# Kernel tuning notes

Hardware: AMD Instinct MI355X
Metric: run time of the kernel (lower is better)

Reference implementation:

```python
import jax, jax.numpy as jnp
import numpy as np


def setup_inputs() -> dict:
    key = jax.random.key(0)
    ks = jax.random.split(key, 8)
    B, T, I, H, O = 4096, 2048, 4, 20, 4
    s_ih = 1.0 / np.sqrt(H)
    return {
        "x": jax.random.normal(ks[0], (B, T, I), dtype=jnp.float32),
        "h0": jax.random.normal(ks[1], (B, H), dtype=jnp.float32),
        "W_ih": jax.random.uniform(ks[2], (H, I), jnp.float32, -s_ih, s_ih),
        "W_hh": jax.random.uniform(ks[3], (H, H), jnp.float32, -s_ih, s_ih),
        "b_ih": jax.random.uniform(ks[4], (H,), jnp.float32, -s_ih, s_ih),
        "b_hh": jax.random.uniform(ks[5], (H,), jnp.float32, -s_ih, s_ih),
        "fc_w": jax.random.uniform(ks[6], (O, H), jnp.float32, -s_ih, s_ih),
        "fc_b": jax.random.uniform(ks[7], (O,), jnp.float32, -s_ih, s_ih),
    }


def reference(x, h0, W_ih, W_hh, b_ih, b_hh, fc_w, fc_b):
    # x: [B, T, I] batch_first; vanilla tanh RNN recurrence.
    # Precompute the input projection for all timesteps in one GEMM.
    xi = jnp.einsum("bti,hi->tbh", x, W_ih) + b_ih + b_hh  # [T, B, H]

    def step(h, xt):
        h = jnp.tanh(xt + h @ W_hh.T)  # [B, H]
        return h, None

    h_last, _ = jax.lax.scan(step, h0, xi)
    # Module takes last timestep only, then Linear(H -> 4).
    return h_last @ fc_w.T + fc_b  # [B, 4]
```

## Files before the change

kernel.cpp:

```cpp
#include <hip/hip_runtime.h>
#include <cstddef>


typedef float f32x2 __attribute__((ext_vector_type(2)));
typedef float f32x4 __attribute__((ext_vector_type(4)));

constexpr int Tn   = 2048;
constexpr int Hn   = 20;
constexpr int EPB  = 16;
constexpr int SB   = 16;
constexpr int NBLK = Tn / SB;

__global__ __launch_bounds__(256, 1) void rnn_fwd(
    const float* __restrict__ x,
    const float* __restrict__ h0,
    const float* __restrict__ W_ih,
    const float* __restrict__ W_hh,
    const float* __restrict__ b_ih,
    const float* __restrict__ b_hh,
    const float* __restrict__ fc_w,
    const float* __restrict__ fc_b,
    float* __restrict__ out)
{
    __shared__ __align__(16) f32x4 xlds[2][EPB][SB + 1];
    __shared__ float hsh[EPB][24];

    const int tid = threadIdx.x;
    const int j   = tid & 15;
    const int e   = tid >> 4;
    const int b   = blockIdx.x * EPB + e;
    const int uB  = 16 + (j & 3);

    const float S = 2.88539008177792681472f;
    const float M = -2.0f * S;

    f32x2 w2[16];
#pragma unroll
    for (int r = 0; r < 16; ++r) {
        const int k = (j - r) & 15;
        w2[r] = f32x2{M * W_hh[j * Hn + k], M * W_hh[uB * Hn + k]};
    }
    f32x2 wqr[4], xiw[4];
#pragma unroll
    for (int c = 0; c < 4; ++c) {
        const int qc = 16 + ((j + c) & 3);
        wqr[c] = f32x2{M * W_hh[j * Hn + qc], M * W_hh[uB * Hn + qc]};
        xiw[c] = f32x2{S * W_ih[j * 4 + c],  S * W_ih[uB * 4 + c]};
    }
    float rsA = 0.0f, rsB = 0.0f;
#pragma unroll
    for (int k = 0; k < Hn; ++k) {
        rsA += W_hh[j  * Hn + k];
        rsB += W_hh[uB * Hn + k];
    }
    f32x2 bias2 = f32x2{S * (b_ih[j]  + b_hh[j]  + rsA),
                        S * (b_ih[uB] + b_hh[uB] + rsB)};

    const float r0A = 0.5f * (1.0f - h0[b * Hn + j]);
    const float r0B = 0.5f * (1.0f - h0[b * Hn + uB]);

    const f32x4* __restrict__ xp =
        reinterpret_cast<const f32x4*>(x) + (size_t)b * Tn;

#define DPPM " row_mask:0xf bank_mask:0xf\n\t"
#define PKB  " op_sel:[0,0,0] op_sel_hi:[1,0,1]\n\t"
#define CLB  "v40","v41","v42","v43","v44","v45","v46","v47","v48","v49",     \
             "v50","v51","v52","v53"

#define STEP_MAC() do {                                                       \
    asm volatile(                                                             \
  "v_pk_fma_f32 %[Q], %[c0], v[44:45], %[Q]" PKB             \
  "v_mov_b32_dpp v42, v44 quad_perm:[1,2,3,0]" DPPM                           \
  "v_pk_fma_f32 %[P], %[w0], v[40:41], %[P]" PKB              \
  "v_mov_b32_dpp v46, v44 quad_perm:[2,3,0,1]" DPPM                           \
  "v_pk_fma_f32 %[Q], %[c1], v[42:43], %[Q]" PKB                              \
  "v_mov_b32_dpp v48, v44 quad_perm:[3,0,1,2]" DPPM                           \
  "v_pk_fma_f32 %[P], %[c2], v[46:47], %[P]" PKB                              \
  "v_mov_b32_dpp v42, v40 row_ror:1"  DPPM                                    \
  "v_pk_fma_f32 %[Q], %[c3], v[48:49], %[Q]" PKB                              \
  "v_mov_b32_dpp v46, v40 row_ror:2"  DPPM                                    \
  "v_pk_fma_f32 %[P], %[w1], v[42:43], %[P]" PKB                              \
  "v_mov_b32_dpp v48, v40 row_ror:3"  DPPM                                    \
  "v_pk_fma_f32 %[Q], %[w2], v[46:47], %[Q]" PKB                              \
  "v_mov_b32_dpp v42, v40 row_ror:4"  DPPM                                    \
  "v_pk_fma_f32 %[P], %[w3], v[48:49], %[P]" PKB                              \
  "v_mov_b32_dpp v46, v40 row_ror:5"  DPPM                                    \
  "v_pk_fma_f32 %[Q], %[w4], v[42:43], %[Q]" PKB                              \
  "v_mov_b32_dpp v48, v40 row_ror:6"  DPPM                                    \
  "v_pk_fma_f32 %[P], %[w5], v[46:47], %[P]" PKB                              \
  "v_mov_b32_dpp v42, v40 row_ror:7"  DPPM                                    \
  "v_pk_fma_f32 %[Q], %[w6], v[48:49], %[Q]" PKB                              \
  "v_mov_b32_dpp v46, v40 row_ror:8"  DPPM                                    \
  "v_pk_fma_f32 %[P], %[w7], v[42:43], %[P]" PKB                              \
  "v_mov_b32_dpp v48, v40 row_ror:9"  DPPM                                    \
  "v_pk_fma_f32 %[Q], %[w8], v[46:47], %[Q]" PKB                              \
  "v_mov_b32_dpp v42, v40 row_ror:10" DPPM                                    \
  "v_pk_fma_f32 %[P], %[w9], v[48:49], %[P]" PKB                              \
  "v_mov_b32_dpp v46, v40 row_ror:11" DPPM                                    \
  "v_pk_fma_f32 %[Q], %[w10], v[42:43], %[Q]" PKB                             \
  "v_mov_b32_dpp v48, v40 row_ror:12" DPPM                                    \
  "v_pk_fma_f32 %[P], %[w11], v[46:47], %[P]" PKB                             \
  "v_mov_b32_dpp v42, v40 row_ror:13" DPPM                                    \
  "v_pk_fma_f32 %[Q], %[w12], v[48:49], %[Q]" PKB                             \
  "v_mov_b32_dpp v46, v40 row_ror:14" DPPM                                    \
  "v_pk_fma_f32 %[P], %[w13], v[42:43], %[P]" PKB                             \
  "v_mov_b32_dpp v48, v40 row_ror:15" DPPM                                    \
  "v_pk_fma_f32 %[Q], %[w14], v[46:47], %[Q]" PKB                             \
  "v_pk_fma_f32 %[P], %[w15], v[48:49], %[P]"                                 \
  " op_sel:[0,0,0] op_sel_hi:[1,0,1]"                                         \
  : [P] "+v"(xiP), [Q] "+v"(xiQ)                                              \
  : [w0] "v"(w2[0]), [w1] "v"(w2[1]),  [w2] "v"(w2[2]),  [w3] "v"(w2[3]),     \
    [w4] "v"(w2[4]), [w5] "v"(w2[5]),  [w6] "v"(w2[6]),  [w7] "v"(w2[7]),     \
    [w8] "v"(w2[8]), [w9] "v"(w2[9]),  [w10] "v"(w2[10]),[w11] "v"(w2[11]),   \
    [w12] "v"(w2[12]),[w13] "v"(w2[13]),[w14] "v"(w2[14]),[w15] "v"(w2[15]),  \
    [c0] "v"(wqr[0]), [c1] "v"(wqr[1]), [c2] "v"(wqr[2]), [c3] "v"(wqr[3])    \
  : CLB);                                                                     \
} while (0)

#define STEP_TAIL(XV) do {                                                    \
    f32x2 xa_ = __builtin_shufflevector((XV), (XV), 0, 1);                    \
    f32x2 xb_ = __builtin_shufflevector((XV), (XV), 2, 3);                    \
    asm volatile(                                                             \
  "v_pk_add_f32 v[50:51], %[P], %[Q]\n\t"                                     \
  "v_pk_fma_f32 %[P], %[x0], %[xa], %[b2]" PKB                                \
  "v_pk_mul_f32 %[Q], %[x1], %[xa] op_sel:[0,1] op_sel_hi:[1,1]\n\t"          \
  "v_exp_f32 v52, v51\n\t"                                                    \
  "v_pk_fma_f32 %[P], %[x2], %[xb], %[P]" PKB                                 \
  "v_exp_f32 v53, v50\n\t"                                                    \
  "v_pk_fma_f32 %[Q], %[x3], %[xb], %[Q] op_sel:[0,1,0] op_sel_hi:[1,1,1]\n\t"\
  "v_add_f32 v52, 1.0, v52\n\t"                                               \
  "v_add_f32 v53, 1.0, v53\n\t"                                               \
  "v_rcp_f32 v44, v52\n\t"                                                    \
  "v_rcp_f32 v40, v53"                                                        \
  : [P] "+v"(xiP), [Q] "+v"(xiQ)                                              \
  : [xa] "v"(xa_), [xb] "v"(xb_),                                             \
    [x0] "v"(xiw[0]), [x1] "v"(xiw[1]), [x2] "v"(xiw[2]), [x3] "v"(xiw[3]),   \
    [b2] "v"(bias2)                                                           \
  : CLB);                                                                     \
} while (0)

#define STEP(XV) do { STEP_MAC(); STEP_TAIL(XV); } while (0)

    xlds[0][e][j] = xp[j];
    f32x4 x0v = xp[0];
    f32x2 xiP, xiQ;
    xiP[0] = __builtin_fmaf(x0v[2], xiw[2][0],
             __builtin_fmaf(x0v[0], xiw[0][0], bias2[0]));
    xiP[1] = __builtin_fmaf(x0v[2], xiw[2][1],
             __builtin_fmaf(x0v[0], xiw[0][1], bias2[1]));
    xiQ[0] = __builtin_fmaf(x0v[3], xiw[3][0], x0v[1] * xiw[1][0]);
    xiQ[1] = __builtin_fmaf(x0v[3], xiw[3][1], x0v[1] * xiw[1][1]);
    asm volatile("v_mov_b32 v40, %0\n\tv_mov_b32 v44, %1"
                 :: "v"(r0A), "v"(r0B) : "v40", "v44");
    f32x4 q0 = xlds[0][e][1];
    f32x4 q1 = xlds[0][e][2];
    f32x4 q2 = xlds[0][e][3];

    int cur = 0;
#pragma unroll 1
    for (int k = 0; k < NBLK; ++k) {
        const int kn = (k + 1 < NBLK) ? (k + 1) : (NBLK - 1);
        f32x4 xr = xp[kn * SB + j];
        const int nxt = cur ^ 1;
#pragma unroll
        for (int s = 0; s < SB - 4; ++s) {
            f32x4 xv = q0; q0 = q1; q1 = q2;
            q2 = xlds[cur][e][s + 4];
            STEP(xv);
        }
        xlds[nxt][e][j] = xr;
        { f32x4 xv = q0; q0 = q1; q1 = q2; q2 = xlds[nxt][e][0]; STEP(xv); }
        { f32x4 xv = q0; q0 = q1; q1 = q2; q2 = xlds[nxt][e][1]; STEP(xv); }
        { f32x4 xv = q0; q0 = q1; q1 = q2; q2 = xlds[nxt][e][2]; STEP(xv); }
        { f32x4 xv = q0; q0 = q1; q1 = q2; q2 = xlds[nxt][e][3]; STEP(xv); }
        cur = nxt;
    }
#undef STEP
#undef STEP_MAC
#undef STEP_TAIL
#undef PKB
#undef DPPM
#undef CLB

    float rAf, rBf;
    asm volatile("v_mov_b32 %0, v40\n\tv_mov_b32 %1, v44"
                 : "=v"(rAf), "=v"(rBf));
    const float hAf = __builtin_fmaf(-2.0f, rAf, 1.0f);
    const float hBf = __builtin_fmaf(-2.0f, rBf, 1.0f);

    hsh[e][j] = hAf;
    if (j < 4) hsh[e][16 + j] = hBf;
    if (j < 4) {
        float o = fc_b[j];
#pragma unroll
        for (int kk = 0; kk < Hn; ++kk)
            o = __builtin_fmaf(hsh[e][kk], fc_w[j * Hn + kk], o);
        out[b * 4 + j] = o;
    }
}

extern "C" void kernel_launch(void* const* d_in, const int* in_sizes, int n_in,
                              void* d_out, int out_size, void* d_ws, size_t ws_size,
                              hipStream_t stream) {
    const float* x    = (const float*)d_in[0];
    const float* h0   = (const float*)d_in[1];
    const float* W_ih = (const float*)d_in[2];
    const float* W_hh = (const float*)d_in[3];
    const float* b_ih = (const float*)d_in[4];
    const float* b_hh = (const float*)d_in[5];
    const float* fc_w = (const float*)d_in[6];
    const float* fc_b = (const float*)d_in[7];
    float* out = (float*)d_out;

    rnn_fwd<<<dim3(256), dim3(256), 0, stream>>>(x, h0, W_ih, W_hh, b_ih, b_hh,
                                                 fc_w, fc_b, out);
}
```

Baseline: 380.8 us.

## Replace LDS-staged x prefetch with per-thread register double buffers

Drops the shared-memory staging of x, where each lane loaded one timestep and others read it from LDS. Every lane now loads all 16 timesteps of its batch element straight from global memory into two 8-entry register buffers, refilled halfway through each block. This removes LDS reads and writes from the serial recurrence. In exchange it costs 16 times more redundant global/L1 loads per lane, adds register pressure, and exposes load latency with only half a block of lookahead. It also fuses the two scalar +1 adds into one packed add.

```diff
diff --git a/kernel.cpp b/kernel.cpp
--- a/kernel.cpp
+++ b/kernel.cpp
@@ -8,8 +8,8 @@
 constexpr int Tn   = 2048;
 constexpr int Hn   = 20;
 constexpr int EPB  = 16;
-constexpr int SB   = 16;
-constexpr int NBLK = Tn / SB;
+constexpr int SPI  = 16;
+constexpr int NIT  = Tn / SPI;
 
 __global__ __launch_bounds__(256, 1) void rnn_fwd(
     const float* __restrict__ x,
@@ -22,7 +22,6 @@
     const float* __restrict__ fc_b,
     float* __restrict__ out)
 {
-    __shared__ __align__(16) f32x4 xlds[2][EPB][SB + 1];
     __shared__ float hsh[EPB][24];
 
     const int tid = threadIdx.x;
@@ -55,6 +54,7 @@
     }
     f32x2 bias2 = f32x2{S * (b_ih[j]  + b_hh[j]  + rsA),
                         S * (b_ih[uB] + b_hh[uB] + rsB)};
+    const f32x2 one2 = f32x2{1.0f, 1.0f};
 
     const float r0A = 0.5f * (1.0f - h0[b * Hn + j]);
     const float r0B = 0.5f * (1.0f - h0[b * Hn + uB]);
@@ -128,21 +128,25 @@
   "v_pk_fma_f32 %[P], %[x2], %[xb], %[P]" PKB                                 \
   "v_exp_f32 v53, v50\n\t"                                                    \
   "v_pk_fma_f32 %[Q], %[x3], %[xb], %[Q] op_sel:[0,1,0] op_sel_hi:[1,1,1]\n\t"\
-  "v_add_f32 v52, 1.0, v52\n\t"                                               \
-  "v_add_f32 v53, 1.0, v53\n\t"                                               \
+  "v_pk_add_f32 v[52:53], v[52:53], %[one]\n\t"                               \
   "v_rcp_f32 v44, v52\n\t"                                                    \
   "v_rcp_f32 v40, v53"                                                        \
   : [P] "+v"(xiP), [Q] "+v"(xiQ)                                              \
   : [xa] "v"(xa_), [xb] "v"(xb_),                                             \
     [x0] "v"(xiw[0]), [x1] "v"(xiw[1]), [x2] "v"(xiw[2]), [x3] "v"(xiw[3]),   \
-    [b2] "v"(bias2)                                                           \
+    [b2] "v"(bias2), [one] "v"(one2)                                          \
   : CLB);                                                                     \
 } while (0)
 
 #define STEP(XV) do { STEP_MAC(); STEP_TAIL(XV); } while (0)
 
-    xlds[0][e][j] = xp[j];
-    f32x4 x0v = xp[0];
+    f32x4 bufA[8], bufB[8];
+#pragma unroll
+    for (int s = 0; s < 8; ++s) bufA[s] = xp[s];
+#pragma unroll
+    for (int s = 0; s < 8; ++s) bufB[s] = xp[8 + s];
+
+    f32x4 x0v = bufA[0];
     f32x2 xiP, xiQ;
     xiP[0] = __builtin_fmaf(x0v[2], xiw[2][0],
              __builtin_fmaf(x0v[0], xiw[0][0], bias2[0]));
@@ -152,28 +156,22 @@
     xiQ[1] = __builtin_fmaf(x0v[3], xiw[3][1], x0v[1] * xiw[1][1]);
     asm volatile("v_mov_b32 v40, %0\n\tv_mov_b32 v44, %1"
                  :: "v"(r0A), "v"(r0B) : "v40", "v44");
-    f32x4 q0 = xlds[0][e][1];
-    f32x4 q1 = xlds[0][e][2];
-    f32x4 q2 = xlds[0][e][3];
-
-    int cur = 0;
+
 #pragma unroll 1
-    for (int k = 0; k < NBLK; ++k) {
-        const int kn = (k + 1 < NBLK) ? (k + 1) : (NBLK - 1);
-        f32x4 xr = xp[kn * SB + j];
-        const int nxt = cur ^ 1;
-#pragma unroll
-        for (int s = 0; s < SB - 4; ++s) {
-            f32x4 xv = q0; q0 = q1; q1 = q2;
-            q2 = xlds[cur][e][s + 4];
-            STEP(xv);
-        }
-        xlds[nxt][e][j] = xr;
-        { f32x4 xv = q0; q0 = q1; q1 = q2; q2 = xlds[nxt][e][0]; STEP(xv); }
-        { f32x4 xv = q0; q0 = q1; q1 = q2; q2 = xlds[nxt][e][1]; STEP(xv); }
-        { f32x4 xv = q0; q0 = q1; q1 = q2; q2 = xlds[nxt][e][2]; STEP(xv); }
-        { f32x4 xv = q0; q0 = q1; q1 = q2; q2 = xlds[nxt][e][3]; STEP(xv); }
-        cur = nxt;
+    for (int k = 0; k < NIT; ++k) {
+        const int kn = (k + 1 < NIT) ? (k + 1) : (NIT - 1);
+        { STEP(bufA[1]); }  { STEP(bufA[2]); }
+        { STEP(bufA[3]); }  { STEP(bufA[4]); }
+        { STEP(bufA[5]); }  { STEP(bufA[6]); }
+        { STEP(bufA[7]); }  { STEP(bufB[0]); }
+#pragma unroll
+        for (int s = 0; s < 8; ++s) bufA[s] = xp[kn * SPI + s];
+        { STEP(bufB[1]); }  { STEP(bufB[2]); }
+        { STEP(bufB[3]); }  { STEP(bufB[4]); }
+        { STEP(bufB[5]); }  { STEP(bufB[6]); }
+        { STEP(bufB[7]); }  { STEP(bufA[0]); }
+#pragma unroll
+        for (int s = 0; s < 8; ++s) bufB[s] = xp[kn * SPI + 8 + s];
     }
 #undef STEP
 #undef STEP_MAC
@@ -190,6 +188,7 @@
 
     hsh[e][j] = hAf;
     if (j < 4) hsh[e][16 + j] = hBf;
+    __builtin_amdgcn_s_waitcnt(0);
     if (j < 4) {
         float o = fc_b[j];
 #pragma unroll
```

Result: faster. 365.6 us (-4.0%).
